# Kernel optimization log

Measured on AMD Instinct MI355X. Metric: run time of the kernel, lower is better.

The kernel has to match this reference:

```python
import jax, jax.numpy as jnp
import numpy as np

C = 256          # in_channels = out_channels per head
H = 4            # heads
NEG_SLOPE = 0.2  # GATConv leaky_relu slope
EPS = 1e-5       # LayerNorm eps
NUM_LAYERS = 2

# fixed 4-node graph: 9 explicit edges + 4 self loops (PyG GATConv default add_self_loops=True)
SRC = jnp.array([1, 1, 2, 2, 3, 3, 1, 2, 3, 0, 1, 2, 3])
DST = jnp.array([2, 3, 1, 3, 1, 2, 0, 0, 0, 0, 1, 2, 3])
ONEHOT = (DST[:, None] == jnp.arange(4)[None, :]).astype(jnp.float32)  # [E=13, N=4]
MASK = ONEHOT.astype(bool)


def gat_layer(x, W, a_src, a_dst, b):
    """PyG GATConv(C, C, heads=4, concat=False), eval mode (no dropout).
    x: [B,4,C]; W: [C, H*C]; a_src/a_dst: [H,C]; b: [C]."""
    B = x.shape[0]
    xp = (x @ W).reshape(B, 4, H, C)                       # [B,4,H,C]
    e_src = jnp.sum(xp * a_src[None, None], axis=-1)       # [B,4,H]
    e_dst = jnp.sum(xp * a_dst[None, None], axis=-1)       # [B,4,H]
    e = jax.nn.leaky_relu(e_src[:, SRC] + e_dst[:, DST], NEG_SLOPE)  # [B,E,H]
    # softmax over incoming edges per destination node (segment softmax, fixed topology)
    m = jnp.max(jnp.where(MASK[None, :, :, None], e[:, :, None, :], -jnp.inf), axis=1)  # [B,4,H]
    ex = jnp.exp(e - m[:, DST])                            # [B,E,H]
    denom = jnp.einsum('beh,ed->bdh', ex, ONEHOT)          # [B,4,H]
    alpha = ex / denom[:, DST]                             # [B,E,H]
    msg = alpha[..., None] * xp[:, SRC]                    # [B,E,H,C]
    out = jnp.einsum('behc,ed->bdhc', msg, ONEHOT)         # [B,4,H,C]
    return out.mean(axis=2) + b                            # concat=False -> head mean, + bias


def layer_norm(x, g, beta):
    mu = jnp.mean(x, axis=-1, keepdims=True)
    var = jnp.mean((x - mu) ** 2, axis=-1, keepdims=True)
    return (x - mu) * jax.lax.rsqrt(var + EPS) * g + beta


def setup_inputs() -> dict:
    key = jax.random.key(0)
    ks = jax.random.split(key, 20)
    B, HW = 32, 64
    inp = {
        'x_ful': jax.random.normal(ks[0], (B, C, HW, HW), jnp.float32),
        'rgb':   jax.random.normal(ks[1], (B, C, HW, HW), jnp.float32),
        'dep':   jax.random.normal(ks[2], (B, C, HW, HW), jnp.float32),
        'tok':   jax.random.normal(ks[3], (1, C), jnp.float32),
    }
    s = 1.0 / np.sqrt(C)
    for i in range(NUM_LAYERS):
        k = jax.random.split(ks[4 + i], 4)
        inp[f'W{i}'] = jax.random.normal(k[0], (C, H * C), jnp.float32) * s
        inp[f'asrc{i}'] = jax.random.normal(k[1], (H, C), jnp.float32) * s
        inp[f'adst{i}'] = jax.random.normal(k[2], (H, C), jnp.float32) * s
        inp[f'b{i}'] = jnp.zeros((C,), jnp.float32)
        inp[f'g{i}'] = jnp.ones((C,), jnp.float32)
        inp[f'beta{i}'] = jnp.zeros((C,), jnp.float32)
    return inp


def reference(x_ful, rgb, dep, tok,
              W0, asrc0, adst0, b0, g0, beta0,
              W1, asrc1, adst1, b1, g1, beta1):
    B = x_ful.shape[0]
    x1 = rgb.mean(axis=(2, 3))    # squeeze_rgb: global avg pool -> [B,C]
    x2 = dep.mean(axis=(2, 3))
    fu = x_ful.mean(axis=(2, 3))
    tokb = jnp.broadcast_to(tok, (B, C))
    nodes = jnp.stack([tokb, fu, x1, x2], axis=1)  # [B,4,C]

    params = [(W0, asrc0, adst0, b0, g0, beta0), (W1, asrc1, adst1, b1, g1, beta1)]
    g = nodes
    for (W, a_s, a_d, b, gam, bet) in params:
        g = gat_layer(g, W, a_s, a_d, b) + g   # residual
        g = layer_norm(g, gam, bet)
        g = jax.nn.relu(g)

    att = jax.nn.sigmoid(g[:, 0, :])[:, :, None, None]  # token node gates channels
    return x_ful * att + x_ful
```

## Files before the change

### kernel.cpp

```cpp
#include <hip/hip_runtime.h>
#include <hip/hip_bf16.h>

#define CCH 256

typedef float f4 __attribute__((ext_vector_type(4)));

__global__ __launch_bounds__(256, 2) void poolA_kernel(
    const float* __restrict__ rgb, const float* __restrict__ dep,
    float* __restrict__ nodes )
{
    const int rw   = blockIdx.x * 4 + (threadIdx.x >> 6);
    const int lane = threadIdx.x & 63;
    const int tensor = rw >> 13;
    const int row    = rw & 8191;
    const f4* src = (const f4*)((tensor ? dep : rgb) + (size_t)row * 4096);

    f4 v[16];
#pragma unroll
    for (int j = 0; j < 16; ++j) v[j] = __builtin_nontemporal_load(src + lane + 64 * j);
    f4 a0 = v[0] + v[1], a1 = v[2] + v[3], a2 = v[4] + v[5], a3 = v[6] + v[7];
    f4 a4 = v[8] + v[9], a5 = v[10] + v[11], a6 = v[12] + v[13], a7 = v[14] + v[15];
    f4 acc = ((a0 + a1) + (a2 + a3)) + ((a4 + a5) + (a6 + a7));

    float s = acc.x + acc.y + acc.z + acc.w;
#pragma unroll
    for (int off = 32; off; off >>= 1) s += __shfl_down(s, off, 64);
    if (lane == 0) {
        const int b = row >> 8, c = row & 255;
        nodes[(size_t)b * 1024 + (2 + tensor) * CCH + c] = s * (1.f / 4096.f);
    }
}

__global__ __launch_bounds__(256, 2) void poolB_kernel(
    const float* __restrict__ xf, float* __restrict__ nodes)
{
    const int row  = blockIdx.x * 4 + (threadIdx.x >> 6);
    const int lane = threadIdx.x & 63;
    const f4* src = (const f4*)(xf + (size_t)row * 4096);

    f4 v[16];
#pragma unroll
    for (int j = 0; j < 16; ++j) v[j] = src[lane + 64 * j];
    f4 a0 = v[0] + v[1], a1 = v[2] + v[3], a2 = v[4] + v[5], a3 = v[6] + v[7];
    f4 a4 = v[8] + v[9], a5 = v[10] + v[11], a6 = v[12] + v[13], a7 = v[14] + v[15];
    f4 acc = ((a0 + a1) + (a2 + a3)) + ((a4 + a5) + (a6 + a7));

    float s = acc.x + acc.y + acc.z + acc.w;
#pragma unroll
    for (int off = 32; off; off >>= 1) s += __shfl_down(s, off, 64);
    if (lane == 0) {
        const int b = row >> 8, c = row & 255;
        nodes[(size_t)b * 1024 + 1 * CCH + c] = s * (1.f / 4096.f);
    }
}

__device__ __forceinline__ void gat_head_core(
    const float X[4][CCH], const float* __restrict__ W,
    const float* __restrict__ As, const float* __restrict__ Ad,
    int h, int c, int lane, int wv,
    float redl[4][8], float esed[8], float alpha_s[4][4],
    float* __restrict__ msg_out )
{
    float acc[4] = {0.f, 0.f, 0.f, 0.f};
    const float* Wp = W + h * 256 + c;
    for (int k0 = 0; k0 < 256; k0 += 16) {
        float wr[16];
#pragma unroll
        for (int u = 0; u < 16; ++u) wr[u] = Wp[(k0 + u) * 1024];
#pragma unroll
        for (int u = 0; u < 16; ++u) {
            float w = wr[u];
            acc[0] += X[0][k0 + u] * w;
            acc[1] += X[1][k0 + u] * w;
            acc[2] += X[2][k0 + u] * w;
            acc[3] += X[3][k0 + u] * w;
        }
    }

    const float av = As[h * 256 + c], dv = Ad[h * 256 + c];
    float rv[8];
#pragma unroll
    for (int n = 0; n < 4; ++n) { rv[n] = acc[n] * av; rv[4 + n] = acc[n] * dv; }
#pragma unroll
    for (int i = 0; i < 8; ++i)
#pragma unroll
        for (int off = 32; off; off >>= 1)
            rv[i] += __shfl_down(rv[i], off, 64);
    if (lane == 0) {
#pragma unroll
        for (int i = 0; i < 8; ++i) redl[wv][i] = rv[i];
    }
    __syncthreads();
    if (c < 8) esed[c] = redl[0][c] + redl[1][c] + redl[2][c] + redl[3][c];
    __syncthreads();

    if (c < 4) {
        const int cnt[4]     = {4, 3, 3, 3};
        const int srcs[4][4] = {{1,2,3,0},{2,3,1,0},{1,3,2,0},{1,2,3,0}};
        const int d = c, n = cnt[d];
        float v[4], m = -1e30f;
        for (int s = 0; s < n; ++s) {
            float e = esed[srcs[d][s]] + esed[4 + d];
            e = (e >= 0.f) ? e : 0.2f * e;
            v[s] = e; m = fmaxf(m, e);
        }
        float den = 0.f;
        for (int s = 0; s < n; ++s) { v[s] = __expf(v[s] - m); den += v[s]; }
        float inv = 1.f / den;
        for (int s = 0; s < n; ++s) alpha_s[d][s] = v[s] * inv;
        for (int s = n; s < 4; ++s) alpha_s[d][s] = 0.f;
    }
    __syncthreads();

    const int srcs2[4][4] = {{1,2,3,0},{2,3,1,0},{1,3,2,0},{1,2,3,0}};
#pragma unroll
    for (int d = 0; d < 4; ++d) {
        float s = 0.f;
#pragma unroll
        for (int sl = 0; sl < 4; ++sl)
            s += alpha_s[d][sl] * acc[srcs2[d][sl]];
        msg_out[d * 256] = s;
    }
}

__global__ __launch_bounds__(256) void gemmA_kernel(
    const float* __restrict__ nodes, const float* __restrict__ tok,
    const float* __restrict__ W0, const float* __restrict__ as0,
    const float* __restrict__ ad0, float* __restrict__ msg1)
{
    const int bid = blockIdx.x, b = bid >> 2, h = bid & 3;
    const int c = threadIdx.x, lane = c & 63, wv = c >> 6;

    __shared__ float X[4][CCH];
    __shared__ float redl[4][8];
    __shared__ float esed[8];
    __shared__ float alpha_s[4][4];

    X[0][c] = tok[c];
    X[1][c] = nodes[b * 1024 + 256 + c];
    X[2][c] = nodes[b * 1024 + 512 + c];
    X[3][c] = nodes[b * 1024 + 768 + c];
    __syncthreads();

    gat_head_core(X, W0, as0, ad0, h, c, lane, wv, redl, esed, alpha_s,
                  msg1 + b * 4096 + h * 1024 + c);
}

__global__ __launch_bounds__(256) void gemmB_kernel(
    const float* __restrict__ nodes, const float* __restrict__ tok,
    const float* __restrict__ msg1,
    const float* __restrict__ b0, const float* __restrict__ g0,
    const float* __restrict__ be0,
    const float* __restrict__ W1, const float* __restrict__ as1,
    const float* __restrict__ ad1, float* __restrict__ msg2)
{
    const int bid = blockIdx.x, b = bid >> 2, h = bid & 3;
    const int c = threadIdx.x, lane = c & 63, wv = c >> 6;

    __shared__ float X[4][CCH];
    __shared__ float redl[4][8];
    __shared__ float esed[8];
    __shared__ float alpha_s[4][4];
    __shared__ float mu_s[4], rstd_s[4];

    const float* m1 = msg1 + b * 4096 + c;
    float gv[4];
#pragma unroll
    for (int d = 0; d < 4; ++d) {
        float s = m1[d * 256] + m1[1024 + d * 256] + m1[2048 + d * 256] + m1[3072 + d * 256];
        float x0 = (d == 0) ? tok[c] : nodes[b * 1024 + d * 256 + c];
        gv[d] = 0.25f * s + b0[c] + x0;
    }
    float rv[8];
#pragma unroll
    for (int d = 0; d < 4; ++d) { rv[d * 2] = gv[d]; rv[d * 2 + 1] = gv[d] * gv[d]; }
#pragma unroll
    for (int i = 0; i < 8; ++i)
#pragma unroll
        for (int off = 32; off; off >>= 1)
            rv[i] += __shfl_down(rv[i], off, 64);
    if (lane == 0) {
#pragma unroll
        for (int i = 0; i < 8; ++i) redl[wv][i] = rv[i];
    }
    __syncthreads();
    if (c < 4) {
        float s = redl[0][c*2]   + redl[1][c*2]   + redl[2][c*2]   + redl[3][c*2];
        float q = redl[0][c*2+1] + redl[1][c*2+1] + redl[2][c*2+1] + redl[3][c*2+1];
        float mu  = s * (1.f / 256.f);
        float var = q * (1.f / 256.f) - mu * mu;
        mu_s[c] = mu; rstd_s[c] = rsqrtf(var + 1e-5f);
    }
    __syncthreads();
    float ga = g0[c], be = be0[c];
#pragma unroll
    for (int d = 0; d < 4; ++d)
        X[d][c] = fmaxf((gv[d] - mu_s[d]) * rstd_s[d] * ga + be, 0.f);
    __syncthreads();

    gat_head_core(X, W1, as1, ad1, h, c, lane, wv, redl, esed, alpha_s,
                  msg2 + b * 4096 + h * 1024 + c);
}

__global__ __launch_bounds__(256) void finish_kernel(
    const float* __restrict__ tok,
    const float* __restrict__ msg1, const float* __restrict__ msg2,
    const float* __restrict__ b0, const float* __restrict__ g0,
    const float* __restrict__ be0,
    const float* __restrict__ b1, const float* __restrict__ g1,
    const float* __restrict__ be1,
    float* __restrict__ scale)
{
    const int b = blockIdx.x, c = threadIdx.x;
    const int lane = c & 63, wv = c >> 6;
    __shared__ float redl[4][2];
    __shared__ float mrs[2];

    const float* m1 = msg1 + b * 4096 + c;
    float gv1 = 0.25f * (m1[0] + m1[1024] + m1[2048] + m1[3072]) + b0[c] + tok[c];
    {
        float s = gv1, q = gv1 * gv1;
#pragma unroll
        for (int off = 32; off; off >>= 1) { s += __shfl_down(s, off, 64); q += __shfl_down(q, off, 64); }
        if (lane == 0) { redl[wv][0] = s; redl[wv][1] = q; }
        __syncthreads();
        if (c == 0) {
            float ss = redl[0][0] + redl[1][0] + redl[2][0] + redl[3][0];
            float qq = redl[0][1] + redl[1][1] + redl[2][1] + redl[3][1];
            float mu = ss * (1.f / 256.f);
            mrs[0] = mu; mrs[1] = rsqrtf(qq * (1.f / 256.f) - mu * mu + 1e-5f);
        }
        __syncthreads();
    }
    float y1 = fmaxf((gv1 - mrs[0]) * mrs[1] * g0[c] + be0[c], 0.f);
    __syncthreads();

    const float* m2 = msg2 + b * 4096 + c;
    float gv2 = 0.25f * (m2[0] + m2[1024] + m2[2048] + m2[3072]) + b1[c] + y1;
    {
        float s = gv2, q = gv2 * gv2;
#pragma unroll
        for (int off = 32; off; off >>= 1) { s += __shfl_down(s, off, 64); q += __shfl_down(q, off, 64); }
        if (lane == 0) { redl[wv][0] = s; redl[wv][1] = q; }
        __syncthreads();
        if (c == 0) {
            float ss = redl[0][0] + redl[1][0] + redl[2][0] + redl[3][0];
            float qq = redl[0][1] + redl[1][1] + redl[2][1] + redl[3][1];
            float mu = ss * (1.f / 256.f);
            mrs[0] = mu; mrs[1] = rsqrtf(qq * (1.f / 256.f) - mu * mu + 1e-5f);
        }
        __syncthreads();
    }
    float y2 = fmaxf((gv2 - mrs[0]) * mrs[1] * g1[c] + be1[c], 0.f);
    scale[b * CCH + c] = 1.f + 1.f / (1.f + __expf(-y2));
}

__global__ __launch_bounds__(256) void apply_kernel(
    const float* __restrict__ xf, const float* __restrict__ scale,
    float* __restrict__ out, int total4)
{
    int idx = blockIdx.x * 256 + threadIdx.x;
    const int stride = gridDim.x * 256;
    const f4* in4 = (const f4*)xf;
    f4* out4 = (f4*)out;
    for (; idx < total4; idx += stride) {
        f4 v = in4[idx];
        const float s = scale[idx >> 10];
        f4 o = v * s;
        __builtin_nontemporal_store(o, out4 + idx);
    }
}

extern "C" void kernel_launch(void* const* d_in, const int* in_sizes, int n_in,
                              void* d_out, int out_size, void* d_ws, size_t ws_size,
                              hipStream_t stream) {
    const float* x_ful = (const float*)d_in[0];
    const float* rgb   = (const float*)d_in[1];
    const float* dep   = (const float*)d_in[2];
    const float* tok   = (const float*)d_in[3];
    const float* W0  = (const float*)d_in[4];
    const float* as0 = (const float*)d_in[5];
    const float* ad0 = (const float*)d_in[6];
    const float* b0  = (const float*)d_in[7];
    const float* g0  = (const float*)d_in[8];
    const float* be0 = (const float*)d_in[9];
    const float* W1  = (const float*)d_in[10];
    const float* as1 = (const float*)d_in[11];
    const float* ad1 = (const float*)d_in[12];
    const float* b1  = (const float*)d_in[13];
    const float* g1  = (const float*)d_in[14];
    const float* be1 = (const float*)d_in[15];

    float* ws    = (float*)d_ws;
    float* nodes = ws;
    float* scale = ws + 32768;
    float* msg1  = ws + 40960;
    float* msg2  = ws + 172032;
    float* out   = (float*)d_out;

    poolA_kernel<<<4096, 256, 0, stream>>>(rgb, dep, nodes);
    poolB_kernel<<<2048, 256, 0, stream>>>(x_ful, nodes);
    gemmA_kernel<<<128, 256, 0, stream>>>(nodes, tok, W0, as0, ad0, msg1);
    gemmB_kernel<<<128, 256, 0, stream>>>(nodes, tok, msg1, b0, g0, be0,
                                          W1, as1, ad1, msg2);
    finish_kernel<<<32, 256, 0, stream>>>(tok, msg1, msg2,
                                          b0, g0, be0, b1, g1, be1, scale);
    const int total4 = 32 * CCH * 64 * 64 / 4;
    apply_kernel<<<2048, 256, 0, stream>>>(x_ful, scale, out, total4);
}
```

Measured before the change: 142.4 us.

## Split GAT GEMM K-dimension across four warp groups and compute only token node in layer 2

The two GAT head kernels now launch 1024 threads per block and split the 256-long reduction dimension into four quarters, combining partial sums through shared memory. This gives more waves to hide the strided weight loads on a grid of only 128 blocks. The second layer now computes attention and messages only for destination node 0 (the token), since only that node feeds the output gate, which shrinks the msg2 writes and the finish kernel's reads. The cost is extra shared memory, extra barriers, and larger blocks that may limit scheduling.

New measurement: 129.0 us. 1.1x faster.

```diff
diff --git a/kernel.cpp b/kernel.cpp
--- a/kernel.cpp
+++ b/kernel.cpp
@@ -54,50 +54,74 @@
     }
 }
 
-__device__ __forceinline__ void gat_head_core(
-    const float X[4][CCH], const float* __restrict__ W,
-    const float* __restrict__ As, const float* __restrict__ Ad,
-    int h, int c, int lane, int wv,
-    float redl[4][8], float esed[8], float alpha_s[4][4],
-    float* __restrict__ msg_out )
-{
+__global__ __launch_bounds__(1024) void gatL0_kernel(
+    const float* __restrict__ nodes, const float* __restrict__ tok,
+    const float* __restrict__ W0, const float* __restrict__ as0,
+    const float* __restrict__ ad0, float* __restrict__ msg1)
+{
+    const int bid = blockIdx.x, b = bid >> 2, h = bid & 3;
+    const int t = threadIdx.x, c = t & 255, kq = t >> 8;
+    const int lane = t & 63, wv = t >> 6;
+
+    __shared__ float X[4][CCH];
+    __shared__ float xpart[3][4][CCH];
+    __shared__ float redl[4][8];
+    __shared__ float esed[8];
+    __shared__ float alpha[4][4];
+
+    X[kq][c] = (kq == 0) ? tok[c] : nodes[(size_t)b * 1024 + kq * 256 + c];
+    __syncthreads();
+
     float acc[4] = {0.f, 0.f, 0.f, 0.f};
-    const float* Wp = W + h * 256 + c;
-    for (int k0 = 0; k0 < 256; k0 += 16) {
+    const float* Wp = W0 + h * 256 + c;
+    const int kb0 = kq * 64;
+    for (int kb = 0; kb < 64; kb += 16) {
         float wr[16];
 #pragma unroll
-        for (int u = 0; u < 16; ++u) wr[u] = Wp[(k0 + u) * 1024];
+        for (int u = 0; u < 16; ++u) wr[u] = Wp[(size_t)(kb0 + kb + u) * 1024];
 #pragma unroll
         for (int u = 0; u < 16; ++u) {
+            const int k = kb0 + kb + u;
             float w = wr[u];
-            acc[0] += X[0][k0 + u] * w;
-            acc[1] += X[1][k0 + u] * w;
-            acc[2] += X[2][k0 + u] * w;
-            acc[3] += X[3][k0 + u] * w;
-        }
-    }
-
-    const float av = As[h * 256 + c], dv = Ad[h * 256 + c];
-    float rv[8];
-#pragma unroll
-    for (int n = 0; n < 4; ++n) { rv[n] = acc[n] * av; rv[4 + n] = acc[n] * dv; }
-#pragma unroll
-    for (int i = 0; i < 8; ++i)
-#pragma unroll
-        for (int off = 32; off; off >>= 1)
-            rv[i] += __shfl_down(rv[i], off, 64);
-    if (lane == 0) {
-#pragma unroll
-        for (int i = 0; i < 8; ++i) redl[wv][i] = rv[i];
-    }
-    __syncthreads();
-    if (c < 8) esed[c] = redl[0][c] + redl[1][c] + redl[2][c] + redl[3][c];
-    __syncthreads();
-
-    if (c < 4) {
+            acc[0] += X[0][k] * w;
+            acc[1] += X[1][k] * w;
+            acc[2] += X[2][k] * w;
+            acc[3] += X[3][k] * w;
+        }
+    }
+    if (kq) {
+#pragma unroll
+        for (int n = 0; n < 4; ++n) xpart[kq - 1][n][c] = acc[n];
+    }
+    __syncthreads();
+
+    if (kq == 0) {
+#pragma unroll
+        for (int n = 0; n < 4; ++n)
+            acc[n] += xpart[0][n][c] + xpart[1][n][c] + xpart[2][n][c];
+
+        const float av = as0[h * 256 + c], dv = ad0[h * 256 + c];
+        float rv[8];
+#pragma unroll
+        for (int n = 0; n < 4; ++n) { rv[n] = acc[n] * av; rv[4 + n] = acc[n] * dv; }
+#pragma unroll
+        for (int i = 0; i < 8; ++i)
+#pragma unroll
+            for (int off = 32; off; off >>= 1)
+                rv[i] += __shfl_down(rv[i], off, 64);
+        if (lane == 0) {
+#pragma unroll
+            for (int i = 0; i < 8; ++i) redl[wv][i] = rv[i];
+        }
+    }
+    __syncthreads();
+    if (t < 8) esed[t] = redl[0][t] + redl[1][t] + redl[2][t] + redl[3][t];
+    __syncthreads();
+
+    if (t < 4) {
         const int cnt[4]     = {4, 3, 3, 3};
         const int srcs[4][4] = {{1,2,3,0},{2,3,1,0},{1,3,2,0},{1,2,3,0}};
-        const int d = c, n = cnt[d];
+        const int d = t, n = cnt[d];
         float v[4], m = -1e30f;
         for (int s = 0; s < n; ++s) {
             float e = esed[srcs[d][s]] + esed[4 + d];
@@ -107,104 +131,143 @@
         float den = 0.f;
         for (int s = 0; s < n; ++s) { v[s] = __expf(v[s] - m); den += v[s]; }
         float inv = 1.f / den;
-        for (int s = 0; s < n; ++s) alpha_s[d][s] = v[s] * inv;
-        for (int s = n; s < 4; ++s) alpha_s[d][s] = 0.f;
-    }
-    __syncthreads();
-
-    const int srcs2[4][4] = {{1,2,3,0},{2,3,1,0},{1,3,2,0},{1,2,3,0}};
-#pragma unroll
-    for (int d = 0; d < 4; ++d) {
-        float s = 0.f;
-#pragma unroll
-        for (int sl = 0; sl < 4; ++sl)
-            s += alpha_s[d][sl] * acc[srcs2[d][sl]];
-        msg_out[d * 256] = s;
-    }
-}
-
-__global__ __launch_bounds__(256) void gemmA_kernel(
-    const float* __restrict__ nodes, const float* __restrict__ tok,
-    const float* __restrict__ W0, const float* __restrict__ as0,
-    const float* __restrict__ ad0, float* __restrict__ msg1)
-{
-    const int bid = blockIdx.x, b = bid >> 2, h = bid & 3;
-    const int c = threadIdx.x, lane = c & 63, wv = c >> 6;
-
-    __shared__ float X[4][CCH];
-    __shared__ float redl[4][8];
-    __shared__ float esed[8];
-    __shared__ float alpha_s[4][4];
-
-    X[0][c] = tok[c];
-    X[1][c] = nodes[b * 1024 + 256 + c];
-    X[2][c] = nodes[b * 1024 + 512 + c];
-    X[3][c] = nodes[b * 1024 + 768 + c];
-    __syncthreads();
-
-    gat_head_core(X, W0, as0, ad0, h, c, lane, wv, redl, esed, alpha_s,
-                  msg1 + b * 4096 + h * 1024 + c);
-}
-
-__global__ __launch_bounds__(256) void gemmB_kernel(
+        for (int s = 0; s < n; ++s) alpha[d][s] = v[s] * inv;
+        for (int s = n; s < 4; ++s) alpha[d][s] = 0.f;
+    }
+    __syncthreads();
+
+    if (kq == 0) {
+        const int srcs2[4][4] = {{1,2,3,0},{2,3,1,0},{1,3,2,0},{1,2,3,0}};
+#pragma unroll
+        for (int d = 0; d < 4; ++d) {
+            float s = 0.f;
+#pragma unroll
+            for (int sl = 0; sl < 4; ++sl)
+                s += alpha[d][sl] * acc[srcs2[d][sl]];
+            msg1[(size_t)b * 4096 + h * 1024 + d * 256 + c] = s;
+        }
+    }
+}
+
+__global__ __launch_bounds__(1024) void gatL1_kernel(
     const float* __restrict__ nodes, const float* __restrict__ tok,
     const float* __restrict__ msg1,
     const float* __restrict__ b0, const float* __restrict__ g0,
     const float* __restrict__ be0,
     const float* __restrict__ W1, const float* __restrict__ as1,
-    const float* __restrict__ ad1, float* __restrict__ msg2)
+    const float* __restrict__ ad1, float* __restrict__ msg2tok)
 {
     const int bid = blockIdx.x, b = bid >> 2, h = bid & 3;
-    const int c = threadIdx.x, lane = c & 63, wv = c >> 6;
+    const int t = threadIdx.x, c = t & 255, kq = t >> 8;
+    const int lane = t & 63, wv = t >> 6;
 
     __shared__ float X[4][CCH];
+    __shared__ float xpart[3][4][CCH];
+    __shared__ float redln[16][2];
+    __shared__ float mu_s[4], rstd_s[4];
     __shared__ float redl[4][8];
     __shared__ float esed[8];
-    __shared__ float alpha_s[4][4];
-    __shared__ float mu_s[4], rstd_s[4];
-
-    const float* m1 = msg1 + b * 4096 + c;
-    float gv[4];
-#pragma unroll
-    for (int d = 0; d < 4; ++d) {
-        float s = m1[d * 256] + m1[1024 + d * 256] + m1[2048 + d * 256] + m1[3072 + d * 256];
-        float x0 = (d == 0) ? tok[c] : nodes[b * 1024 + d * 256 + c];
-        gv[d] = 0.25f * s + b0[c] + x0;
-    }
-    float rv[8];
-#pragma unroll
-    for (int d = 0; d < 4; ++d) { rv[d * 2] = gv[d]; rv[d * 2 + 1] = gv[d] * gv[d]; }
-#pragma unroll
-    for (int i = 0; i < 8; ++i)
-#pragma unroll
-        for (int off = 32; off; off >>= 1)
-            rv[i] += __shfl_down(rv[i], off, 64);
-    if (lane == 0) {
-#pragma unroll
-        for (int i = 0; i < 8; ++i) redl[wv][i] = rv[i];
-    }
-    __syncthreads();
-    if (c < 4) {
-        float s = redl[0][c*2]   + redl[1][c*2]   + redl[2][c*2]   + redl[3][c*2];
-        float q = redl[0][c*2+1] + redl[1][c*2+1] + redl[2][c*2+1] + redl[3][c*2+1];
-        float mu  = s * (1.f / 256.f);
-        float var = q * (1.f / 256.f) - mu * mu;
-        mu_s[c] = mu; rstd_s[c] = rsqrtf(var + 1e-5f);
-    }
-    __syncthreads();
-    float ga = g0[c], be = be0[c];
-#pragma unroll
-    for (int d = 0; d < 4; ++d)
-        X[d][c] = fmaxf((gv[d] - mu_s[d]) * rstd_s[d] * ga + be, 0.f);
-    __syncthreads();
-
-    gat_head_core(X, W1, as1, ad1, h, c, lane, wv, redl, esed, alpha_s,
-                  msg2 + b * 4096 + h * 1024 + c);
+    __shared__ float alpha[4][4];
+
+    {
+        const float* m1 = msg1 + (size_t)b * 4096 + kq * 256 + c;
+        float s = m1[0] + m1[1024] + m1[2048] + m1[3072];
+        float x0 = (kq == 0) ? tok[c] : nodes[(size_t)b * 1024 + kq * 256 + c];
+        float gv = 0.25f * s + b0[c] + x0;
+        float ss = gv, qq = gv * gv;
+#pragma unroll
+        for (int off = 32; off; off >>= 1) {
+            ss += __shfl_down(ss, off, 64);
+            qq += __shfl_down(qq, off, 64);
+        }
+        if (lane == 0) { redln[wv][0] = ss; redln[wv][1] = qq; }
+        __syncthreads();
+        if (t < 4) {
+            float s4 = redln[4*t][0] + redln[4*t+1][0] + redln[4*t+2][0] + redln[4*t+3][0];
+            float q4 = redln[4*t][1] + redln[4*t+1][1] + redln[4*t+2][1] + redln[4*t+3][1];
+            float mu  = s4 * (1.f / 256.f);
+            float var = q4 * (1.f / 256.f) - mu * mu;
+            mu_s[t] = mu; rstd_s[t] = rsqrtf(var + 1e-5f);
+        }
+        __syncthreads();
+        X[kq][c] = fmaxf((gv - mu_s[kq]) * rstd_s[kq] * g0[c] + be0[c], 0.f);
+    }
+    __syncthreads();
+
+    float acc[4] = {0.f, 0.f, 0.f, 0.f};
+    const float* Wp = W1 + h * 256 + c;
+    const int kb0 = kq * 64;
+    for (int kb = 0; kb < 64; kb += 16) {
+        float wr[16];
+#pragma unroll
+        for (int u = 0; u < 16; ++u) wr[u] = Wp[(size_t)(kb0 + kb + u) * 1024];
+#pragma unroll
+        for (int u = 0; u < 16; ++u) {
+            const int k = kb0 + kb + u;
+            float w = wr[u];
+            acc[0] += X[0][k] * w;
+            acc[1] += X[1][k] * w;
+            acc[2] += X[2][k] * w;
+            acc[3] += X[3][k] * w;
+        }
+    }
+    if (kq) {
+#pragma unroll
+        for (int n = 0; n < 4; ++n) xpart[kq - 1][n][c] = acc[n];
+    }
+    __syncthreads();
+
+    if (kq == 0) {
+#pragma unroll
+        for (int n = 0; n < 4; ++n)
+            acc[n] += xpart[0][n][c] + xpart[1][n][c] + xpart[2][n][c];
+
+        const float av = as1[h * 256 + c], dv = ad1[h * 256 + c];
+        float rv[8];
+#pragma unroll
+        for (int n = 0; n < 4; ++n) { rv[n] = acc[n] * av; rv[4 + n] = acc[n] * dv; }
+#pragma unroll
+        for (int i = 0; i < 8; ++i)
+#pragma unroll
+            for (int off = 32; off; off >>= 1)
+                rv[i] += __shfl_down(rv[i], off, 64);
+        if (lane == 0) {
+#pragma unroll
+            for (int i = 0; i < 8; ++i) redl[wv][i] = rv[i];
+        }
+    }
+    __syncthreads();
+    if (t < 8) esed[t] = redl[0][t] + redl[1][t] + redl[2][t] + redl[3][t];
+    __syncthreads();
+
+    if (t == 0) {
+        const int srcs0[4] = {1, 2, 3, 0};
+        float v[4], m = -1e30f;
+        for (int s = 0; s < 4; ++s) {
+            float e = esed[srcs0[s]] + esed[4];
+            e = (e >= 0.f) ? e : 0.2f * e;
+            v[s] = e; m = fmaxf(m, e);
+        }
+        float den = 0.f;
+        for (int s = 0; s < 4; ++s) { v[s] = __expf(v[s] - m); den += v[s]; }
+        float inv = 1.f / den;
+        for (int s = 0; s < 4; ++s) alpha[0][s] = v[s] * inv;
+    }
+    __syncthreads();
+
+    if (kq == 0) {
+        const int srcs0[4] = {1, 2, 3, 0};
+        float s = 0.f;
+#pragma unroll
+        for (int sl = 0; sl < 4; ++sl)
+            s += alpha[0][sl] * acc[srcs0[sl]];
+        msg2tok[(size_t)b * 1024 + h * 256 + c] = s;
+    }
 }
 
 __global__ __launch_bounds__(256) void finish_kernel(
     const float* __restrict__ tok,
-    const float* __restrict__ msg1, const float* __restrict__ msg2,
+    const float* __restrict__ msg1, const float* __restrict__ msg2tok,
     const float* __restrict__ b0, const float* __restrict__ g0,
     const float* __restrict__ be0,
     const float* __restrict__ b1, const float* __restrict__ g1,
@@ -216,7 +279,7 @@
     __shared__ float redl[4][2];
     __shared__ float mrs[2];
 
-    const float* m1 = msg1 + b * 4096 + c;
+    const float* m1 = msg1 + (size_t)b * 4096 + c;
     float gv1 = 0.25f * (m1[0] + m1[1024] + m1[2048] + m1[3072]) + b0[c] + tok[c];
     {
         float s = gv1, q = gv1 * gv1;
@@ -235,8 +298,8 @@
     float y1 = fmaxf((gv1 - mrs[0]) * mrs[1] * g0[c] + be0[c], 0.f);
     __syncthreads();
 
-    const float* m2 = msg2 + b * 4096 + c;
-    float gv2 = 0.25f * (m2[0] + m2[1024] + m2[2048] + m2[3072]) + b1[c] + y1;
+    const float* m2 = msg2tok + (size_t)b * 1024 + c;
+    float gv2 = 0.25f * (m2[0] + m2[256] + m2[512] + m2[768]) + b1[c] + y1;
     {
         float s = gv2, q = gv2 * gv2;
 #pragma unroll
@@ -252,7 +315,7 @@
         __syncthreads();
     }
     float y2 = fmaxf((gv2 - mrs[0]) * mrs[1] * g1[c] + be1[c], 0.f);
-    scale[b * CCH + c] = 1.f + 1.f / (1.f + __expf(-y2));
+    scale[(size_t)b * CCH + c] = 1.f + 1.f / (1.f + __expf(-y2));
 }
 
 __global__ __launch_bounds__(256) void apply_kernel(
@@ -291,19 +354,19 @@
     const float* g1  = (const float*)d_in[14];
     const float* be1 = (const float*)d_in[15];
 
-    float* ws    = (float*)d_ws;
-    float* nodes = ws;
-    float* scale = ws + 32768;
-    float* msg1  = ws + 40960;
-    float* msg2  = ws + 172032;
-    float* out   = (float*)d_out;
+    float* ws      = (float*)d_ws;
+    float* nodes   = ws;
+    float* scale   = ws + 32768;
+    float* msg1    = ws + 40960;
+    float* msg2tok = ws + 172032;
+    float* out     = (float*)d_out;
 
     poolA_kernel<<<4096, 256, 0, stream>>>(rgb, dep, nodes);
     poolB_kernel<<<2048, 256, 0, stream>>>(x_ful, nodes);
-    gemmA_kernel<<<128, 256, 0, stream>>>(nodes, tok, W0, as0, ad0, msg1);
-    gemmB_kernel<<<128, 256, 0, stream>>>(nodes, tok, msg1, b0, g0, be0,
-                                          W1, as1, ad1, msg2);
-    finish_kernel<<<32, 256, 0, stream>>>(tok, msg1, msg2,
+    gatL0_kernel<<<128, 1024, 0, stream>>>(nodes, tok, W0, as0, ad0, msg1);
+    gatL1_kernel<<<128, 1024, 0, stream>>>(nodes, tok, msg1, b0, g0, be0,
+                                           W1, as1, ad1, msg2tok);
+    finish_kernel<<<32, 256, 0, stream>>>(tok, msg1, msg2tok,
                                           b0, g0, be0, b1, g1, be1, scale);
     const int total4 = 32 * CCH * 64 * 64 / 4;
     apply_kernel<<<2048, 256, 0, stream>>>(x_ful, scale, out, total4);
```
